# Kernel optimization log

Measured on AMD Instinct MI355X. Metric: run time of the kernel, lower is better.

The kernel has to match this reference:

```python
import jax, jax.numpy as jnp
import numpy as np

N_NODES = 100000

def _sage_conv(x, src, dst, W_l, b_l, W_r):
    # PyG SAGEConv(aggr='mean'): out = lin_l(mean_{j in N(i)} x_j) + lin_r(x_i)
    agg = jax.ops.segment_sum(x[src], dst, num_segments=N_NODES)          # [N, F]
    cnt = jax.ops.segment_sum(jnp.ones_like(dst, dtype=x.dtype), dst,
                              num_segments=N_NODES)                        # [N]
    mean = agg / jnp.maximum(cnt, 1.0)[:, None]
    return mean @ W_l + b_l + x @ W_r

def setup_inputs() -> dict:
    key = jax.random.key(0)
    ks = jax.random.split(key, 10)
    F_in, H = 128, 16
    E, P = 1600000, 2000000
    x = jax.random.normal(ks[0], (N_NODES, F_in), dtype=jnp.float32)
    edge_index = jax.random.randint(ks[1], (2, E), 0, N_NODES, dtype=jnp.int64)
    decode_index = jax.random.randint(ks[2], (2, P), 0, N_NODES, dtype=jnp.int64)
    s1 = 1.0 / np.sqrt(F_in)
    s2 = 1.0 / np.sqrt(H)
    W1l = jax.random.uniform(ks[3], (F_in, H), jnp.float32, -s1, s1)
    b1 = jax.random.uniform(ks[4], (H,), jnp.float32, -s1, s1)
    W1r = jax.random.uniform(ks[5], (F_in, H), jnp.float32, -s1, s1)
    W2l = jax.random.uniform(ks[6], (H, H), jnp.float32, -s2, s2)
    b2 = jax.random.uniform(ks[7], (H,), jnp.float32, -s2, s2)
    W2r = jax.random.uniform(ks[8], (H, H), jnp.float32, -s2, s2)
    return {"x": x, "W1l": W1l, "b1": b1, "W1r": W1r,
            "W2l": W2l, "b2": b2, "W2r": W2r,
            "edge_index": edge_index, "decode_index": decode_index}

def reference(x, W1l, b1, W1r, W2l, b2, W2r, edge_index, decode_index):
    src, dst = edge_index[0], edge_index[1]
    h = _sage_conv(x, src, dst, W1l, b1, W1r)          # conv1
    h = jax.nn.relu(h)                                  # relu (dropout: eval -> identity)
    h = _sage_conv(h, src, dst, W2l, b2, W2r)           # conv2
    logits = jnp.sum(h[decode_index[0]] * h[decode_index[1]], axis=1)  # [P]
    return jax.nn.sigmoid(logits)
```

## Files before the change

kernel.cpp:

```cpp
#include <hip/hip_runtime.h>
#include <hip/hip_fp16.h>

#define N_NODES 100000
#define F_IN 128
#define H 16
#define NBIN 391
#define BINCAP 4608
#define ECHUNK 8192
#define QSCALE 4096.0f
#define QINV (1.0f / 4096.0f)

__device__ inline unsigned int packi16(float a, float b) {
  int ia = __float2int_rn(fminf(fmaxf(a * QSCALE, -32767.f), 32767.f));
  int ib = __float2int_rn(fminf(fmaxf(b * QSCALE, -32767.f), 32767.f));
  return (unsigned int)((ia & 0xffff) | (ib << 16));
}

__global__ void __launch_bounds__(512) k_init(int* __restrict__ binCur) {
  int t = threadIdx.x;
  if (t < NBIN) binCur[t] = t * BINCAP;
}

__global__ void __launch_bounds__(256) k_lin1(
    const float* __restrict__ x, const float* __restrict__ W1l,
    const float* __restrict__ W1r, unsigned short* __restrict__ y1l,
    float* __restrict__ y1r) {
  __shared__ float red[3 * 32 * 64];
  int t = threadIdx.x;
  int part = __builtin_amdgcn_readfirstlane(t >> 6);
  int ln = t & 63;
  int n = blockIdx.x * 64 + ln;
  int nc = (n < N_NODES) ? n : (N_NODES - 1);
  const float4* xr = (const float4*)(x + (size_t)nc * F_IN + part * (F_IN / 4));
  float4 xv[8];
#pragma unroll
  for (int j = 0; j < 8; ++j) xv[j] = xr[j];
  const float* Wl = W1l + part * (F_IN / 4) * H;
  const float* Wr = W1r + part * (F_IN / 4) * H;
  float al[H], ar[H];
#pragma unroll
  for (int c = 0; c < H; ++c) { al[c] = 0.f; ar[c] = 0.f; }
#pragma unroll
  for (int j = 0; j < 8; ++j) {
    float xs[4] = {xv[j].x, xv[j].y, xv[j].z, xv[j].w};
#pragma unroll
    for (int jj = 0; jj < 4; ++jj) {
      int k = j * 4 + jj;
#pragma unroll
      for (int c = 0; c < H; ++c) {
        al[c] = fmaf(xs[jj], Wl[k * H + c], al[c]);
        ar[c] = fmaf(xs[jj], Wr[k * H + c], ar[c]);
      }
    }
  }
  if (part != 0) {
    int base = (part - 1) * 2048;
#pragma unroll
    for (int c = 0; c < H; ++c) {
      red[base + c * 64 + ln] = al[c];
      red[base + (H + c) * 64 + ln] = ar[c];
    }
  }
  __syncthreads();
  if (part == 0 && n < N_NODES) {
#pragma unroll
    for (int c = 0; c < H; ++c) {
      al[c] = ((al[c] + red[c * 64 + ln]) + red[2048 + c * 64 + ln])
              + red[4096 + c * 64 + ln];
      ar[c] = ((ar[c] + red[(H + c) * 64 + ln]) + red[2048 + (H + c) * 64 + ln])
              + red[4096 + (H + c) * 64 + ln];
    }
    uint4 w0, w1;
    w0.x = packi16(al[0], al[1]);  w0.y = packi16(al[2], al[3]);
    w0.z = packi16(al[4], al[5]);  w0.w = packi16(al[6], al[7]);
    w1.x = packi16(al[8], al[9]);  w1.y = packi16(al[10], al[11]);
    w1.z = packi16(al[12], al[13]); w1.w = packi16(al[14], al[15]);
    uint4* ol = (uint4*)(y1l + (size_t)n * H);
    ol[0] = w0;
    ol[1] = w1;
    float4* orr = (float4*)(y1r + (size_t)n * H);
#pragma unroll
    for (int q = 0; q < 4; ++q)
      orr[q] = make_float4(ar[4 * q], ar[4 * q + 1], ar[4 * q + 2], ar[4 * q + 3]);
  }
}

__global__ void __launch_bounds__(512) k_binfill(
    const int* __restrict__ src, const int* __restrict__ dst,
    int* __restrict__ binCur, int* __restrict__ recs, int E) {
  __shared__ int hist[512];
  __shared__ int gbase[512];
  __shared__ int cnt2[512];
  int t = threadIdx.x;
  hist[t] = 0;
  cnt2[t] = 0;
  __syncthreads();
  int base = blockIdx.x * ECHUNK;
  int rec[16], bin[16];
#pragma unroll
  for (int j = 0; j < 16; ++j) {
    int e = base + j * 512 + t;
    if (e < E) {
      int s = src[e];
      int d = dst[e];
      rec[j] = (s << 8) | (d & 255);
      bin[j] = d >> 8;
      atomicAdd(&hist[bin[j]], 1);
    } else {
      bin[j] = -1;
    }
  }
  __syncthreads();
  if (t < NBIN) {
    int c = hist[t];
    gbase[t] = (c > 0) ? atomicAdd(&binCur[t], c) : 0;
  }
  __syncthreads();
#pragma unroll
  for (int j = 0; j < 16; ++j) {
    if (bin[j] >= 0) {
      int loc = atomicAdd(&cnt2[bin[j]], 1);
      int slot = gbase[bin[j]] + loc;
      if (slot < (bin[j] + 1) * BINCAP)
        recs[slot] = rec[j];
    }
  }
}

__global__ void __launch_bounds__(512) k_group(
    int* __restrict__ recs, const int* __restrict__ binCur,
    int* __restrict__ deg, int* __restrict__ rowBeg) {
  __shared__ int lrec[BINCAP];
  __shared__ int hist[256];
  __shared__ int off[256];
  __shared__ int cur[256];
  int t = threadIdx.x;
  int b = blockIdx.x;
  int rbase = b * BINCAP;
  int R = binCur[b] - rbase;
  if (R > BINCAP) R = BINCAP;
  if (t < 256) hist[t] = 0;
  __syncthreads();
#pragma unroll
  for (int j = 0; j < 9; ++j) {
    int idx = j * 512 + t;
    if (idx < R) {
      int r = recs[rbase + idx];
      lrec[idx] = r;
      atomicAdd(&hist[r & 255], 1);
    }
  }
  __syncthreads();
  if (t < 256) off[t] = hist[t];
  __syncthreads();
  for (int o = 1; o < 256; o <<= 1) {
    int u = 0;
    if (t < 256 && t >= o) u = off[t - o];
    __syncthreads();
    if (t < 256) off[t] += u;
    __syncthreads();
  }
  if (t < 256) {
    int ex = off[t] - hist[t];
    cur[t] = ex;
    int n = (b << 8) + t;
    if (n < N_NODES) {
      deg[n] = hist[t];
      rowBeg[n] = rbase + ex;
    }
  }
  __syncthreads();
#pragma unroll
  for (int j = 0; j < 9; ++j) {
    int idx = j * 512 + t;
    if (idx < R) {
      int r = lrec[idx];
      int slot = atomicAdd(&cur[r & 255], 1);
      recs[rbase + slot] = r >> 8;
    }
  }
}

__global__ void __launch_bounds__(256) k_gather1(
    const int* __restrict__ srcSorted, const int* __restrict__ deg,
    const int* __restrict__ rowBeg, const unsigned short* __restrict__ y1l,
    const float* __restrict__ y1r, const float* __restrict__ b1,
    const float* __restrict__ W2l, const float* __restrict__ W2r,
    unsigned short* __restrict__ z2l, float* __restrict__ z2r) {
  int tid = blockIdx.x * 256 + threadIdx.x;
  int n = tid >> 2;
  int q = tid & 3;
  if (n >= N_NODES) return;
  int beg = rowBeg[n];
  int dg = deg[n];
  int end = beg + dg;
  int acc0 = 0, acc1 = 0, acc2 = 0, acc3 = 0;
  int i = beg;
  for (; i + 8 <= end; i += 8) {
    int sqa = srcSorted[i + q];
    int sqb = srcSorted[i + 4 + q];
#pragma unroll
    for (int j = 0; j < 4; ++j) {
      int sa = __shfl(sqa, j, 4);
      int sb = __shfl(sqb, j, 4);
      uint2 va = *(const uint2*)(y1l + (size_t)sa * H + q * 4);
      uint2 vb = *(const uint2*)(y1l + (size_t)sb * H + q * 4);
      acc0 += (((int)(va.x << 16)) >> 16) + (((int)(vb.x << 16)) >> 16);
      acc1 += (((int)va.x) >> 16) + (((int)vb.x) >> 16);
      acc2 += (((int)(va.y << 16)) >> 16) + (((int)(vb.y << 16)) >> 16);
      acc3 += (((int)va.y) >> 16) + (((int)vb.y) >> 16);
    }
  }
  for (; i + 4 <= end; i += 4) {
    int sq = srcSorted[i + q];
#pragma unroll
    for (int j = 0; j < 4; ++j) {
      int sj = __shfl(sq, j, 4);
      uint2 v = *(const uint2*)(y1l + (size_t)sj * H + q * 4);
      acc0 += ((int)(v.x << 16)) >> 16;
      acc1 += ((int)v.x) >> 16;
      acc2 += ((int)(v.y << 16)) >> 16;
      acc3 += ((int)v.y) >> 16;
    }
  }
  for (; i < end; ++i) {
    int sj = srcSorted[i];
    uint2 v = *(const uint2*)(y1l + (size_t)sj * H + q * 4);
    acc0 += ((int)(v.x << 16)) >> 16;
    acc1 += ((int)v.x) >> 16;
    acc2 += ((int)(v.y << 16)) >> 16;
    acc3 += ((int)v.y) >> 16;
  }
  float s = (1.f / fmaxf((float)dg, 1.f)) * QINV;
  float4 yr = *(const float4*)(y1r + (size_t)n * H + q * 4);
  float4 bb = *(const float4*)(b1 + q * 4);
  float h1x = fmaxf(fmaf((float)acc0, s, bb.x + yr.x), 0.f);
  float h1y = fmaxf(fmaf((float)acc1, s, bb.y + yr.y), 0.f);
  float h1z = fmaxf(fmaf((float)acc2, s, bb.z + yr.z), 0.f);
  float h1w = fmaxf(fmaf((float)acc3, s, bb.w + yr.w), 0.f);
  float zl0 = 0.f, zl1 = 0.f, zl2 = 0.f, zl3 = 0.f;
  float zr0 = 0.f, zr1 = 0.f, zr2 = 0.f, zr3 = 0.f;
#pragma unroll
  for (int sl = 0; sl < 4; ++sl) {
    float hx = __shfl(h1x, sl, 4);
    float hy = __shfl(h1y, sl, 4);
    float hz = __shfl(h1z, sl, 4);
    float hw = __shfl(h1w, sl, 4);
    float hk4[4] = {hx, hy, hz, hw};
#pragma unroll
    for (int j = 0; j < 4; ++j) {
      int k = sl * 4 + j;
      float4 wl = *(const float4*)(W2l + k * H + q * 4);
      float4 wr = *(const float4*)(W2r + k * H + q * 4);
      float hk = hk4[j];
      zl0 = fmaf(hk, wl.x, zl0); zl1 = fmaf(hk, wl.y, zl1);
      zl2 = fmaf(hk, wl.z, zl2); zl3 = fmaf(hk, wl.w, zl3);
      zr0 = fmaf(hk, wr.x, zr0); zr1 = fmaf(hk, wr.y, zr1);
      zr2 = fmaf(hk, wr.z, zr2); zr3 = fmaf(hk, wr.w, zr3);
    }
  }
  uint2 pk;
  pk.x = packi16(zl0, zl1);
  pk.y = packi16(zl2, zl3);
  *(uint2*)(z2l + (size_t)n * H + q * 4) = pk;
  *(float4*)(z2r + (size_t)n * H + q * 4) = make_float4(zr0, zr1, zr2, zr3);
}

__global__ void __launch_bounds__(256) k_gather2(
    const int* __restrict__ srcSorted, const int* __restrict__ deg,
    const int* __restrict__ rowBeg, const unsigned short* __restrict__ z2l,
    const float* __restrict__ z2r, const float* __restrict__ b2,
    __half* __restrict__ h2) {
  int tid = blockIdx.x * 256 + threadIdx.x;
  int n = tid >> 2;
  int q = tid & 3;
  if (n >= N_NODES) return;
  int beg = rowBeg[n];
  int dg = deg[n];
  int end = beg + dg;
  int acc0 = 0, acc1 = 0, acc2 = 0, acc3 = 0;
  int i = beg;
  for (; i + 8 <= end; i += 8) {
    int sqa = srcSorted[i + q];
    int sqb = srcSorted[i + 4 + q];
#pragma unroll
    for (int j = 0; j < 4; ++j) {
      int sa = __shfl(sqa, j, 4);
      int sb = __shfl(sqb, j, 4);
      uint2 va = *(const uint2*)(z2l + (size_t)sa * H + q * 4);
      uint2 vb = *(const uint2*)(z2l + (size_t)sb * H + q * 4);
      acc0 += (((int)(va.x << 16)) >> 16) + (((int)(vb.x << 16)) >> 16);
      acc1 += (((int)va.x) >> 16) + (((int)vb.x) >> 16);
      acc2 += (((int)(va.y << 16)) >> 16) + (((int)(vb.y << 16)) >> 16);
      acc3 += (((int)va.y) >> 16) + (((int)vb.y) >> 16);
    }
  }
  for (; i + 4 <= end; i += 4) {
    int sq = srcSorted[i + q];
#pragma unroll
    for (int j = 0; j < 4; ++j) {
      int sj = __shfl(sq, j, 4);
      uint2 v = *(const uint2*)(z2l + (size_t)sj * H + q * 4);
      acc0 += ((int)(v.x << 16)) >> 16;
      acc1 += ((int)v.x) >> 16;
      acc2 += ((int)(v.y << 16)) >> 16;
      acc3 += ((int)v.y) >> 16;
    }
  }
  for (; i < end; ++i) {
    int sj = srcSorted[i];
    uint2 v = *(const uint2*)(z2l + (size_t)sj * H + q * 4);
    acc0 += ((int)(v.x << 16)) >> 16;
    acc1 += ((int)v.x) >> 16;
    acc2 += ((int)(v.y << 16)) >> 16;
    acc3 += ((int)v.y) >> 16;
  }
  float s = (1.f / fmaxf((float)dg, 1.f)) * QINV;
  float4 zr = *(const float4*)(z2r + (size_t)n * H + q * 4);
  float4 bb = *(const float4*)(b2 + q * 4);
  float v0 = fmaf((float)acc0, s, bb.x + zr.x);
  float v1 = fmaf((float)acc1, s, bb.y + zr.y);
  float v2 = fmaf((float)acc2, s, bb.z + zr.z);
  float v3 = fmaf((float)acc3, s, bb.w + zr.w);
  __half2 h0 = __floats2half2_rn(v0, v1);
  __half2 h1 = __floats2half2_rn(v2, v3);
  uint2 pk;
  pk.x = *(unsigned int*)&h0;
  pk.y = *(unsigned int*)&h1;
  *(uint2*)(h2 + (size_t)n * H + q * 4) = pk;
}

__device__ inline float dot8h(uint4 u, uint4 v) {
  float acc = 0.f;
  const unsigned int* uw = (const unsigned int*)&u;
  const unsigned int* vw = (const unsigned int*)&v;
#pragma unroll
  for (int j = 0; j < 4; ++j) {
    float2 a = __half22float2(*(const __half2*)&uw[j]);
    float2 b = __half22float2(*(const __half2*)&vw[j]);
    acc = fmaf(a.x, b.x, acc);
    acc = fmaf(a.y, b.y, acc);
  }
  return acc;
}

__global__ void __launch_bounds__(256) k_decode(
    const int* __restrict__ ps, const int* __restrict__ pd,
    const __half* __restrict__ h2, float* __restrict__ out, int P) {
  int t = blockIdx.x * 256 + threadIdx.x;
  int p = t * 2;
  if (p >= P) return;
  int2 av = *(const int2*)(ps + p);
  int2 bv = *(const int2*)(pd + p);
  const uint4* ha0 = (const uint4*)(h2 + (size_t)av.x * H);
  const uint4* hb0 = (const uint4*)(h2 + (size_t)bv.x * H);
  const uint4* ha1 = (const uint4*)(h2 + (size_t)av.y * H);
  const uint4* hb1 = (const uint4*)(h2 + (size_t)bv.y * H);
  uint4 u00 = ha0[0], u01 = ha0[1];
  uint4 v00 = hb0[0], v01 = hb0[1];
  uint4 u10 = ha1[0], u11 = ha1[1];
  uint4 v10 = hb1[0], v11 = hb1[1];
  float d0 = dot8h(u00, v00) + dot8h(u01, v01);
  float d1 = dot8h(u10, v10) + dot8h(u11, v11);
  float o0 = 1.f / (1.f + __expf(-d0));
  float o1 = 1.f / (1.f + __expf(-d1));
  if (p + 1 < P) {
    *(float2*)(out + p) = make_float2(o0, o1);
  } else {
    out[p] = o0;
  }
}

extern "C" void kernel_launch(void* const* d_in, const int* in_sizes, int n_in,
                              void* d_out, int out_size, void* d_ws, size_t ws_size,
                              hipStream_t stream) {
  const float* x   = (const float*)d_in[0];
  const float* W1l = (const float*)d_in[1];
  const float* b1  = (const float*)d_in[2];
  const float* W1r = (const float*)d_in[3];
  const float* W2l = (const float*)d_in[4];
  const float* b2  = (const float*)d_in[5];
  const float* W2r = (const float*)d_in[6];
  const int* ei = (const int*)d_in[7];
  const int* di = (const int*)d_in[8];
  const int E = in_sizes[7] / 2;
  const int P = in_sizes[8] / 2;

  const size_t NF = (size_t)N_NODES * H;
  unsigned short* y1l = (unsigned short*)d_ws;
  __half*         h2  = (__half*)y1l;
  unsigned short* z2l = y1l + NF;
  float*  y1r = (float*)(z2l + NF);
  float*  z2r = y1r;
  int* recs   = (int*)(y1r + NF);
  int* binCur = recs + (size_t)NBIN * BINCAP;
  int* deg    = binCur + 512;
  int* rowBeg = deg + N_NODES;

  const int lin1Blocks = (N_NODES + 63) / 64;
  const int fillBlocks = (E + ECHUNK - 1) / ECHUNK;
  const int gatherBlocks = ((N_NODES * 4) + 255) / 256;
  const int decodeBlocks = ((P + 1) / 2 + 255) / 256;

  k_init<<<1, 512, 0, stream>>>(binCur);
  k_lin1<<<lin1Blocks, 256, 0, stream>>>(x, W1l, W1r, y1l, y1r);
  k_binfill<<<fillBlocks, 512, 0, stream>>>(ei, ei + E, binCur, recs, E);
  k_group<<<NBIN, 512, 0, stream>>>(recs, binCur, deg, rowBeg);
  k_gather1<<<gatherBlocks, 256, 0, stream>>>(recs, deg, rowBeg, y1l, y1r,
                                              b1, W2l, W2r, z2l, z2r);
  k_gather2<<<gatherBlocks, 256, 0, stream>>>(recs, deg, rowBeg, z2l, z2r,
                                              b2, h2);
  k_decode<<<decodeBlocks, 256, 0, stream>>>(di, di + P, h2, (float*)d_out, P);
}
```

Before: 213.6 us.

## Sort nodes by degree bucket and widen gather index loads

Adds a per-node degree histogram in the grouping kernel, plus two small kernels that prefix-scan the histogram and build a permutation grouping nodes of similar degree. Both gather kernels now process nodes in that permuted order, so each wavefront covers nodes with similar edge counts and less work is lost to divergence. The main gather loop also loads 16 source indices at once with one int4 load per lane and spreads them with shuffles. In exchange it adds two kernel launches, random-order reads of rowBeg and deg, scattered output writes, and int4 index loads that may be unaligned.

```diff
diff --git a/kernel.cpp b/kernel.cpp
--- a/kernel.cpp
+++ b/kernel.cpp
@@ -7,6 +7,7 @@
 #define NBIN 391
 #define BINCAP 4608
 #define ECHUNK 8192
+#define NDBUCKET 64
 #define QSCALE 4096.0f
 #define QINV (1.0f / 4096.0f)
 
@@ -16,9 +17,11 @@
   return (unsigned int)((ia & 0xffff) | (ib << 16));
 }
 
-__global__ void __launch_bounds__(512) k_init(int* __restrict__ binCur) {
+__global__ void __launch_bounds__(512) k_init(int* __restrict__ binCur,
+                                              int* __restrict__ degHist) {
   int t = threadIdx.x;
   if (t < NBIN) binCur[t] = t * BINCAP;
+  if (t < NDBUCKET) degHist[t] = 0;
 }
 
 __global__ void __launch_bounds__(256) k_lin1(
@@ -129,17 +132,20 @@
 
 __global__ void __launch_bounds__(512) k_group(
     int* __restrict__ recs, const int* __restrict__ binCur,
-    int* __restrict__ deg, int* __restrict__ rowBeg) {
+    int* __restrict__ deg, int* __restrict__ rowBeg,
+    int* __restrict__ degHist) {
   __shared__ int lrec[BINCAP];
   __shared__ int hist[256];
   __shared__ int off[256];
   __shared__ int cur[256];
+  __shared__ int dh[NDBUCKET];
   int t = threadIdx.x;
   int b = blockIdx.x;
   int rbase = b * BINCAP;
   int R = binCur[b] - rbase;
   if (R > BINCAP) R = BINCAP;
   if (t < 256) hist[t] = 0;
+  if (t >= 256 && t < 256 + NDBUCKET) dh[t - 256] = 0;
   __syncthreads();
 #pragma unroll
   for (int j = 0; j < 9; ++j) {
@@ -167,9 +173,12 @@
     if (n < N_NODES) {
       deg[n] = hist[t];
       rowBeg[n] = rbase + ex;
-    }
-  }
-  __syncthreads();
+      int bk = hist[t] < NDBUCKET ? hist[t] : (NDBUCKET - 1);
+      atomicAdd(&dh[bk], 1);
+    }
+  }
+  __syncthreads();
+  if (t < NDBUCKET && dh[t] > 0) atomicAdd(&degHist[t], dh[t]);
 #pragma unroll
   for (int j = 0; j < 9; ++j) {
     int idx = j * 512 + t;
@@ -181,34 +190,61 @@
   }
 }
 
+__global__ void __launch_bounds__(64) k_pscan(
+    const int* __restrict__ degHist, int* __restrict__ degCur) {
+  __shared__ int s[NDBUCKET];
+  int t = threadIdx.x;
+  int v = degHist[t];
+  s[t] = v;
+  __syncthreads();
+  for (int o = 1; o < NDBUCKET; o <<= 1) {
+    int u = (t >= o) ? s[t - o] : 0;
+    __syncthreads();
+    s[t] += u;
+    __syncthreads();
+  }
+  degCur[t] = s[t] - v;
+}
+
+__global__ void __launch_bounds__(256) k_pfill(
+    const int* __restrict__ deg, int* __restrict__ degCur,
+    int* __restrict__ perm) {
+  int n = blockIdx.x * 256 + threadIdx.x;
+  if (n >= N_NODES) return;
+  int d = deg[n];
+  int bk = d < NDBUCKET ? d : (NDBUCKET - 1);
+  int slot = atomicAdd(&degCur[bk], 1);
+  perm[slot] = n;
+}
+
 __global__ void __launch_bounds__(256) k_gather1(
-    const int* __restrict__ srcSorted, const int* __restrict__ deg,
-    const int* __restrict__ rowBeg, const unsigned short* __restrict__ y1l,
-    const float* __restrict__ y1r, const float* __restrict__ b1,
-    const float* __restrict__ W2l, const float* __restrict__ W2r,
-    unsigned short* __restrict__ z2l, float* __restrict__ z2r) {
+    const int* __restrict__ perm, const int* __restrict__ srcSorted,
+    const int* __restrict__ deg, const int* __restrict__ rowBeg,
+    const unsigned short* __restrict__ y1l, const float* __restrict__ y1r,
+    const float* __restrict__ b1, const float* __restrict__ W2l,
+    const float* __restrict__ W2r, unsigned short* __restrict__ z2l,
+    float* __restrict__ z2r) {
   int tid = blockIdx.x * 256 + threadIdx.x;
-  int n = tid >> 2;
+  int g = tid >> 2;
   int q = tid & 3;
-  if (n >= N_NODES) return;
+  if (g >= N_NODES) return;
+  int n = perm[g];
   int beg = rowBeg[n];
   int dg = deg[n];
   int end = beg + dg;
   int acc0 = 0, acc1 = 0, acc2 = 0, acc3 = 0;
   int i = beg;
-  for (; i + 8 <= end; i += 8) {
-    int sqa = srcSorted[i + q];
-    int sqb = srcSorted[i + 4 + q];
-#pragma unroll
-    for (int j = 0; j < 4; ++j) {
-      int sa = __shfl(sqa, j, 4);
-      int sb = __shfl(sqb, j, 4);
-      uint2 va = *(const uint2*)(y1l + (size_t)sa * H + q * 4);
-      uint2 vb = *(const uint2*)(y1l + (size_t)sb * H + q * 4);
-      acc0 += (((int)(va.x << 16)) >> 16) + (((int)(vb.x << 16)) >> 16);
-      acc1 += (((int)va.x) >> 16) + (((int)vb.x) >> 16);
-      acc2 += (((int)(va.y << 16)) >> 16) + (((int)(vb.y << 16)) >> 16);
-      acc3 += (((int)va.y) >> 16) + (((int)vb.y) >> 16);
+  for (; i + 16 <= end; i += 16) {
+    int4 iv = *(const int4*)(srcSorted + i + q * 4);
+    int vj[4] = {iv.x, iv.y, iv.z, iv.w};
+#pragma unroll
+    for (int j = 0; j < 16; ++j) {
+      int sj = __shfl(vj[j & 3], j >> 2, 4);
+      uint2 v = *(const uint2*)(y1l + (size_t)sj * H + q * 4);
+      acc0 += ((int)(v.x << 16)) >> 16;
+      acc1 += ((int)v.x) >> 16;
+      acc2 += ((int)(v.y << 16)) >> 16;
+      acc3 += ((int)v.y) >> 16;
     }
   }
   for (; i + 4 <= end; i += 4) {
@@ -267,32 +303,31 @@
 }
 
 __global__ void __launch_bounds__(256) k_gather2(
-    const int* __restrict__ srcSorted, const int* __restrict__ deg,
-    const int* __restrict__ rowBeg, const unsigned short* __restrict__ z2l,
-    const float* __restrict__ z2r, const float* __restrict__ b2,
-    __half* __restrict__ h2) {
+    const int* __restrict__ perm, const int* __restrict__ srcSorted,
+    const int* __restrict__ deg, const int* __restrict__ rowBeg,
+    const unsigned short* __restrict__ z2l, const float* __restrict__ z2r,
+    const float* __restrict__ b2, __half* __restrict__ h2) {
   int tid = blockIdx.x * 256 + threadIdx.x;
-  int n = tid >> 2;
+  int g = tid >> 2;
   int q = tid & 3;
-  if (n >= N_NODES) return;
+  if (g >= N_NODES) return;
+  int n = perm[g];
   int beg = rowBeg[n];
   int dg = deg[n];
   int end = beg + dg;
   int acc0 = 0, acc1 = 0, acc2 = 0, acc3 = 0;
   int i = beg;
-  for (; i + 8 <= end; i += 8) {
-    int sqa = srcSorted[i + q];
-    int sqb = srcSorted[i + 4 + q];
-#pragma unroll
-    for (int j = 0; j < 4; ++j) {
-      int sa = __shfl(sqa, j, 4);
-      int sb = __shfl(sqb, j, 4);
-      uint2 va = *(const uint2*)(z2l + (size_t)sa * H + q * 4);
-      uint2 vb = *(const uint2*)(z2l + (size_t)sb * H + q * 4);
-      acc0 += (((int)(va.x << 16)) >> 16) + (((int)(vb.x << 16)) >> 16);
-      acc1 += (((int)va.x) >> 16) + (((int)vb.x) >> 16);
-      acc2 += (((int)(va.y << 16)) >> 16) + (((int)(vb.y << 16)) >> 16);
-      acc3 += (((int)va.y) >> 16) + (((int)vb.y) >> 16);
+  for (; i + 16 <= end; i += 16) {
+    int4 iv = *(const int4*)(srcSorted + i + q * 4);
+    int vj[4] = {iv.x, iv.y, iv.z, iv.w};
+#pragma unroll
+    for (int j = 0; j < 16; ++j) {
+      int sj = __shfl(vj[j & 3], j >> 2, 4);
+      uint2 v = *(const uint2*)(z2l + (size_t)sj * H + q * 4);
+      acc0 += ((int)(v.x << 16)) >> 16;
+      acc1 += ((int)v.x) >> 16;
+      acc2 += ((int)(v.y << 16)) >> 16;
+      acc3 += ((int)v.y) >> 16;
     }
   }
   for (; i + 4 <= end; i += 4) {
@@ -392,23 +427,30 @@
   unsigned short* z2l = y1l + NF;
   float*  y1r = (float*)(z2l + NF);
   float*  z2r = y1r;
-  int* recs   = (int*)(y1r + NF);
-  int* binCur = recs + (size_t)NBIN * BINCAP;
-  int* deg    = binCur + 512;
-  int* rowBeg = deg + N_NODES;
+  int* recs    = (int*)(y1r + NF);
+  int* binCur  = recs + (size_t)NBIN * BINCAP;
+  int* deg     = binCur + 512;
+  int* rowBeg  = deg + N_NODES;
+  int* degHist = rowBeg + N_NODES;
+  int* degCur  = degHist + NDBUCKET;
+  int* perm    = degCur + NDBUCKET;
 
   const int lin1Blocks = (N_NODES + 63) / 64;
   const int fillBlocks = (E + ECHUNK - 1) / ECHUNK;
+  const int nodeBlocks = (N_NODES + 255) / 256;
   const int gatherBlocks = ((N_NODES * 4) + 255) / 256;
   const int decodeBlocks = ((P + 1) / 2 + 255) / 256;
 
-  k_init<<<1, 512, 0, stream>>>(binCur);
+  k_init<<<1, 512, 0, stream>>>(binCur, degHist);
   k_lin1<<<lin1Blocks, 256, 0, stream>>>(x, W1l, W1r, y1l, y1r);
   k_binfill<<<fillBlocks, 512, 0, stream>>>(ei, ei + E, binCur, recs, E);
-  k_group<<<NBIN, 512, 0, stream>>>(recs, binCur, deg, rowBeg);
-  k_gather1<<<gatherBlocks, 256, 0, stream>>>(recs, deg, rowBeg, y1l, y1r,
-                                              b1, W2l, W2r, z2l, z2r);
-  k_gather2<<<gatherBlocks, 256, 0, stream>>>(recs, deg, rowBeg, z2l, z2r,
-                                              b2, h2);
+  k_group<<<NBIN, 512, 0, stream>>>(recs, binCur, deg, rowBeg, degHist);
+  k_pscan<<<1, 64, 0, stream>>>(degHist, degCur);
+  k_pfill<<<nodeBlocks, 256, 0, stream>>>(deg, degCur, perm);
+  k_gather1<<<gatherBlocks, 256, 0, stream>>>(perm, recs, deg, rowBeg,
+                                              y1l, y1r, b1, W2l, W2r,
+                                              z2l, z2r);
+  k_gather2<<<gatherBlocks, 256, 0, stream>>>(perm, recs, deg, rowBeg,
+                                              z2l, z2r, b2, h2);
   k_decode<<<decodeBlocks, 256, 0, stream>>>(di, di + P, h2, (float*)d_out, P);
 }
```

New measurement: 491.8 us. 130% more time.
